# Performance work log

Measured on AMD Instinct MI355X. Metric: run time of the kernel, lower is better.

Reference implementation:

```python
import jax, jax.numpy as jnp
import numpy as np

B = 32
T, F1, F2 = 128, 8, 8          # input_shape
N_PATCHES = 1024               # (128/4)*(8/1)*(8/2)
INPUT_D = 8                    # 4*1*2
D = 64                         # hidden_d
H = 8                          # n_heads
DH = D // H                    # d_head = 8
S = N_PATCHES + 1              # sequence length with class token
OUT_D = 9
EPS = 1e-5


def _pos_emb(seq_len, d):
    # Faithful to the original (including the odd-index formula precedence):
    # even j: sin(i / 10000**(j/d));  odd j: cos(i / (10000**(j-1) / d))
    i = np.arange(seq_len, dtype=np.float64)[:, None]
    j = np.arange(d, dtype=np.float64)[None, :]
    even = np.sin(i / np.power(10000.0, j / d))
    odd = np.cos(i / (np.power(10000.0, j - 1.0) / d))
    return jnp.asarray(np.where(j.astype(np.int64) % 2 == 0, even, odd), dtype=jnp.float32)


def _layernorm2d(x, gamma, beta):
    # nn.LayerNorm((S, D)): normalize over the last TWO dims, affine [S, D]
    mu = jnp.mean(x, axis=(-2, -1), keepdims=True)
    var = jnp.mean((x - mu) ** 2, axis=(-2, -1), keepdims=True)
    return (x - mu) * jax.lax.rsqrt(var + EPS) * gamma + beta


def setup_inputs() -> dict:
    key = jax.random.key(0)
    ks = jax.random.split(key, 18)
    sc = 0.05
    return {
        "images": jax.random.normal(ks[0], (B, T, F1, F2), jnp.float32),
        "w_map": jax.random.normal(ks[1], (INPUT_D, D), jnp.float32) * sc,
        "b_map": jax.random.normal(ks[2], (D,), jnp.float32) * sc,
        "cls_tok": jax.random.uniform(ks[3], (1, D), jnp.float32),
        "g1": jnp.ones((S, D), jnp.float32),
        "be1": jnp.zeros((S, D), jnp.float32),
        "wq": jax.random.normal(ks[4], (H, DH, DH), jnp.float32) * sc,
        "bq": jax.random.normal(ks[5], (H, DH), jnp.float32) * sc,
        "wk": jax.random.normal(ks[6], (H, DH, DH), jnp.float32) * sc,
        "bk": jax.random.normal(ks[7], (H, DH), jnp.float32) * sc,
        "wv": jax.random.normal(ks[8], (H, DH, DH), jnp.float32) * sc,
        "bv": jax.random.normal(ks[9], (H, DH), jnp.float32) * sc,
        "g2": jnp.ones((S, D), jnp.float32),
        "be2": jnp.zeros((S, D), jnp.float32),
        "w_enc": jax.random.normal(ks[10], (D, D), jnp.float32) * sc,
        "b_enc": jax.random.normal(ks[11], (D,), jnp.float32) * sc,
        "w_out": jax.random.normal(ks[12], (D, OUT_D), jnp.float32) * sc,
        "b_out": jax.random.normal(ks[13], (OUT_D,), jnp.float32) * sc,
    }


def _msa(x, wq, bq, wk, bk, wv, bv):
    # x: [B, S, D] -> per-head linear QKV, softmax attention, concat heads
    b, s, _ = x.shape
    xh = x.reshape(b, s, H, DH)                                   # [B,S,H,dh]
    q = jnp.einsum("bshd,hde->bshe", xh, wq) + bq
    k = jnp.einsum("bshd,hde->bshe", xh, wk) + bk
    v = jnp.einsum("bshd,hde->bshe", xh, wv) + bv
    scores = jnp.einsum("bqhe,bkhe->bhqk", q, k) / (DH ** 0.5)    # [B,H,S,S]
    attn = jax.nn.softmax(scores, axis=-1)
    out = jnp.einsum("bhqk,bkhe->bqhe", attn, v)                  # [B,S,H,dh]
    return out.reshape(b, s, D)


def reference(images, w_map, b_map, cls_tok, g1, be1, wq, bq, wk, bk, wv, bv,
              g2, be2, w_enc, b_enc, w_out, b_out):
    n = images.shape[0]
    patches = images.reshape(n, N_PATCHES, INPUT_D)
    tokens = patches @ w_map + b_map                              # [B,P,D]
    cls = jnp.broadcast_to(cls_tok[None, :, :], (n, 1, D))
    tokens = jnp.concatenate([cls, tokens], axis=1)               # [B,S,D]
    tokens = tokens + _pos_emb(S, D)[None, :, :]
    out = tokens + _msa(_layernorm2d(tokens, g1, be1), wq, bq, wk, bk, wv, bv)
    out = out + jax.nn.relu(_layernorm2d(out, g2, be2) @ w_enc + b_enc)
    h = out[:, 0]                                                 # class token
    return jax.nn.softmax(h @ w_out + b_out, axis=-1)
```

## Files before the change

### kernel.cpp

```cpp
#include <hip/hip_runtime.h>
#include <math.h>

#define BB 32
#define SS 1025
#define DD 64
#define HH 8
#define IN_D 8
#define NPATCH 1024
#define OUTD 9
#define EPSF 1e-5f
#define SD (SS*DD)
#define SP 1056
#define NQT 65
#define NCH 33
#define VTROW 1064
#define PSTR 40
#define NTB 257
#define ZROW 1055

typedef __attribute__((ext_vector_type(8))) short bf16x8;
typedef __attribute__((ext_vector_type(4))) float f32x4;

#define SCALE_LOG2E (0.35355339059327378f * 1.4426950408889634f)

#if __has_builtin(__builtin_amdgcn_exp2f)
__device__ __forceinline__ float exp2_fast(float x) { return __builtin_amdgcn_exp2f(x); }
#else
__device__ __forceinline__ float exp2_fast(float x) {
    float r; asm("v_exp_f32 %0, %1" : "=v"(r) : "v"(x)); return r;
}
#endif

__device__ __forceinline__ short f2bf(float f) {
    union { float f; unsigned u; } a; a.f = f;
    unsigned r = a.u + 0x7FFFu + ((a.u >> 16) & 1u);
    return (short)(r >> 16);
}
__device__ __forceinline__ unsigned pack_bf16x2(float lo, float hi) {
    unsigned ul = __float_as_uint(lo) + 0x8000u;
    unsigned uh = __float_as_uint(hi) + 0x8000u;
    return __builtin_amdgcn_perm(uh, ul, 0x07060302u);
}

__device__ __forceinline__ int sigma32(int k) {
    return 16 * (k & 1) + 4 * (k >> 3) + ((k >> 1) & 3);
}

__global__ void k_tokens(const float* __restrict__ images, const float* __restrict__ w_map,
                         const float* __restrict__ b_map, const float* __restrict__ cls,
                         float* __restrict__ tokens, float* __restrict__ part1,
                         float* __restrict__ partq1, float* __restrict__ sum2,
                         float* __restrict__ sumsq2) {
    int b = blockIdx.y;
    int bx = blockIdx.x;
    int idx = bx * 256 + threadIdx.x;
    int tid = threadIdx.x;
    __shared__ float recip[64];
    __shared__ float sh[512];
    if (tid < 64) {
        int j = tid;
        float div;
        if ((j & 1) == 0)
            div = powf(10000.0f, (float)j * (1.0f / 64.0f));
        else
            div = powf(10000.0f, (float)(j - 1)) * (1.0f / 64.0f);
        recip[j] = 1.0f / div;
    }
    __syncthreads();
    float lv = 0.f, lvv = 0.f;
    if (idx < SD) {
        int s = idx >> 6, j = idx & 63;
        float arg = (float)s * recip[j];
        float pv = (j & 1) ? __cosf(arg) : __sinf(arg);
        float v;
        if (s == 0) {
            v = cls[j];
        } else {
            const float* p = images + (size_t)b * (NPATCH * IN_D) + (size_t)(s - 1) * IN_D;
            float acc = b_map[j];
#pragma unroll
            for (int i = 0; i < IN_D; ++i) acc += p[i] * w_map[i * DD + j];
            v = acc;
        }
        v += pv;
        tokens[(size_t)b * SD + idx] = v;
        lv = v; lvv = v * v;
    }
    sh[tid] = lv; sh[256 + tid] = lvv;
    __syncthreads();
    for (int off = 128; off > 0; off >>= 1) {
        if (tid < off) { sh[tid] += sh[tid + off]; sh[256 + tid] += sh[256 + tid + off]; }
        __syncthreads();
    }
    if (tid == 0) {
        part1[b * NTB + bx] = sh[0];
        partq1[b * NTB + bx] = sh[256];
    }
    if (bx == 0) {
        if (tid == 0) sum2[b] = 0.f;
        if (tid == 1) sumsq2[b] = 0.f;
    }
}

__global__ void k_qkv(const float* __restrict__ tokens, const float* __restrict__ part1,
                      const float* __restrict__ partq1, const float* __restrict__ g1,
                      const float* __restrict__ be1,
                      const float* __restrict__ wq, const float* __restrict__ bq,
                      const float* __restrict__ wk, const float* __restrict__ bk,
                      const float* __restrict__ wv, const float* __restrict__ bv,
                      short* __restrict__ qb, short* __restrict__ kb, short* __restrict__ vb) {
    int b = blockIdx.y, bx = blockIdx.x, tid = threadIdx.x;
    __shared__ float sh[512];
    __shared__ float xs[4][DD];
    __shared__ float stats[2];
    {
        float s = 0.f, ss = 0.f;
        for (int i = tid; i < NTB; i += 256) { s += part1[b * NTB + i]; ss += partq1[b * NTB + i]; }
        sh[tid] = s; sh[256 + tid] = ss;
        __syncthreads();
        for (int off = 128; off > 0; off >>= 1) {
            if (tid < off) { sh[tid] += sh[tid + off]; sh[256 + tid] += sh[256 + tid + off]; }
            __syncthreads();
        }
        if (tid == 0) {
            float mu = sh[0] / (float)SD;
            float var = sh[256] / (float)SD - mu * mu;
            stats[0] = mu;
            stats[1] = rsqrtf(var + EPSF);
        }
        __syncthreads();
    }
    int r = tid >> 6, d = tid & 63;
    int srow = bx * 4 + r;
    if (srow < SS) {
        float t = tokens[((size_t)b * SS + srow) * DD + d];
        xs[r][d] = (t - stats[0]) * stats[1] * g1[srow * DD + d] + be1[srow * DD + d];
    }
    __syncthreads();
    for (int o = tid; o < 768; o += 256) {
        int rr = o / 192;
        int rem = o % 192;
        int which = rem / 64;
        int he = rem % 64;
        int h = he >> 3, e = he & 7;
        int s2 = bx * 4 + rr;
        if (s2 >= SS) continue;
        const float* w = (which == 0) ? wq : (which == 1) ? wk : wv;
        const float* bias = (which == 0) ? bq : (which == 1) ? bk : bv;
        float acc = bias[he];
#pragma unroll
        for (int dd = 0; dd < 8; ++dd)
            acc += xs[rr][h * 8 + dd] * w[(h * 8 + dd) * 8 + e];
        if (which == 0) acc *= SCALE_LOG2E;
        short* dst = (which == 0) ? qb : (which == 1) ? kb : vb;
        dst[((size_t)(b * HH + h) * SP + s2) * 8 + e] = f2bf(acc);
    }
    if (bx == NTB - 1) {
        for (int i = tid; i < (SP - SS) * HH * 8; i += 256) {
            int rr = i / (HH * 8);
            int he = i % (HH * 8);
            int hh = he >> 3, e = he & 7;
            kb[((size_t)(b * HH + hh) * SP + SS + rr) * 8 + e] = 0;
        }
    }
}

__global__ __launch_bounds__(512, 6)
void k_attn(const short* __restrict__ qb, const short* __restrict__ kb, const short* __restrict__ vb,
            const float* __restrict__ tokens, float* __restrict__ out0,
            float* __restrict__ sum2, float* __restrict__ sumsq2) {
    __shared__ __align__(16) short VTs[9 * VTROW];
    __shared__ __align__(16) short Ps[8 * 2 * 16 * PSTR];
    int h = blockIdx.y, b = blockIdx.z;
    int bh = b * HH + h;
    int tid = threadIdx.x;
    int wave = tid >> 6, lane = tid & 63;
    int col = lane & 15, quad = lane >> 4;

    bf16x8 z8 = {0, 0, 0, 0, 0, 0, 0, 0};
    {
        const bf16x8* vg = (const bf16x8*)(vb + (size_t)bh * SP * 8);
        for (int i = tid; i < SP; i += 512) {
            int t = (i & ~31) | sigma32(i & 31);
            if (t < SS) {
                bf16x8 row = vg[t];
#pragma unroll
                for (int e = 0; e < 8; ++e) VTs[e * VTROW + i] = row[e];
                VTs[8 * VTROW + i] = (short)0x3F80;
            } else {
#pragma unroll
                for (int e = 0; e < 9; ++e) VTs[e * VTROW + i] = 0;
            }
        }
    }
    __syncthreads();

    const short* kg = kb + (size_t)bh * SP * 8;
    const short* kp0 = kg + ((quad == 0) ? col * 8 : ZROW * 8);
    const int kstep = (quad == 0) ? 256 : 0;
    const int koff16 = (quad == 0) ? 128 : 0;
    const short* vbase_l = VTs + (col < 9 ? col : 8) * VTROW + quad * 8;
    short* pbase = Ps + wave * (2 * 16 * PSTR);
    short* pwr = pbase + (quad * 4) * PSTR + 2 * col;
    const short* prd = pbase + col * PSTR + quad * 8;

    float lsum = 0.f, lssq = 0.f;
    int slot = blockIdx.x * 8 + wave;

    for (int qt = slot; qt < NQT; qt += 24) {
        bf16x8 qfrag = z8;
        if (quad == 0) qfrag = *(const bf16x8*)(qb + ((size_t)bh * SP + qt * 16 + col) * 8);
        f32x4 o = {0.f, 0.f, 0.f, 0.f};
        const f32x4 zz = {0.f, 0.f, 0.f, 0.f};
        const short* kptr = kp0;
        bf16x8 ka = *(const bf16x8*)kptr;
        bf16x8 kb_ = *(const bf16x8*)(kptr + koff16);
        {
            f32x4 s0 = __builtin_amdgcn_mfma_f32_16x16x32_bf16(qfrag, ka, zz, 0, 0, 0);
            f32x4 s1 = __builtin_amdgcn_mfma_f32_16x16x32_bf16(qfrag, kb_, zz, 0, 0, 0);
#pragma unroll
            for (int r = 0; r < 4; ++r)
                *(unsigned*)(pwr + r * PSTR) = pack_bf16x2(exp2_fast(s0[r]), exp2_fast(s1[r]));
        }
        for (int ch = 0; ch < NCH; ++ch) {
            bf16x8 pf = *(const bf16x8*)(prd + (ch & 1) * (16 * PSTR));
            bf16x8 vf = *(const bf16x8*)(vbase_l + ch * 32);
            if (ch + 1 < NCH) {
                kptr += kstep;
                ka = *(const bf16x8*)kptr;
                kb_ = *(const bf16x8*)(kptr + koff16);
                f32x4 s0 = __builtin_amdgcn_mfma_f32_16x16x32_bf16(qfrag, ka, zz, 0, 0, 0);
                f32x4 s1 = __builtin_amdgcn_mfma_f32_16x16x32_bf16(qfrag, kb_, zz, 0, 0, 0);
                short* pw = pwr + ((ch + 1) & 1) * (16 * PSTR);
#pragma unroll
                for (int r = 0; r < 4; ++r)
                    *(unsigned*)(pw + r * PSTR) = pack_bf16x2(exp2_fast(s0[r]), exp2_fast(s1[r]));
            }
            o = __builtin_amdgcn_mfma_f32_16x16x32_bf16(pf, vf, o, 0, 0, 0);
        }
        float* Pf = (float*)pbase;
#pragma unroll
        for (int r = 0; r < 4; ++r) Pf[(quad * 4 + r) * 16 + col] = o[r];
#pragma unroll
        for (int pass = 0; pass < 2; ++pass) {
            int idx = lane + pass * 64;
            int qq = idx >> 3, e = idx & 7;
            int qg = qt * 16 + qq;
            if (qg < SS) {
                float num = Pf[qq * 16 + e];
                float l = Pf[qq * 16 + 8];
                float ov = tokens[((size_t)b * SS + qg) * DD + h * 8 + e] + num / l;
                lsum += ov; lssq += ov * ov;
                if (qg == 0) out0[b * DD + h * 8 + e] = ov;
            }
        }
    }

    __syncthreads();
    float* red = (float*)Ps;
    red[tid] = lsum; red[512 + tid] = lssq;
    __syncthreads();
    for (int off = 256; off > 0; off >>= 1) {
        if (tid < off) { red[tid] += red[tid + off]; red[512 + tid] += red[512 + tid + off]; }
        __syncthreads();
    }
    if (tid == 0) {
        atomicAdd(&sum2[b], red[0]);
        atomicAdd(&sumsq2[b], red[512]);
    }
}

__global__ void k_final(const float* __restrict__ out0, const float* __restrict__ sum2,
                        const float* __restrict__ sumsq2, const float* __restrict__ g2,
                        const float* __restrict__ be2, const float* __restrict__ w_enc,
                        const float* __restrict__ b_enc, const float* __restrict__ w_out,
                        const float* __restrict__ b_out, float* __restrict__ out) {
    int b = blockIdx.x;
    int tid = threadIdx.x;
    __shared__ float xn[DD], hsh[DD], logit[OUTD];
    float n = (float)SD;
    float mu = sum2[b] / n;
    float var = sumsq2[b] / n - mu * mu;
    float rs = rsqrtf(var + EPSF);
    float o = out0[b * DD + tid];
    xn[tid] = (o - mu) * rs * g2[tid] + be2[tid];
    __syncthreads();
    float acc = b_enc[tid];
#pragma unroll
    for (int d = 0; d < DD; ++d) acc += xn[d] * w_enc[d * DD + tid];
    hsh[tid] = o + fmaxf(acc, 0.f);
    __syncthreads();
    if (tid < OUTD) {
        float a = b_out[tid];
#pragma unroll
        for (int d = 0; d < DD; ++d) a += hsh[d] * w_out[d * OUTD + tid];
        logit[tid] = a;
    }
    __syncthreads();
    if (tid == 0) {
        float m = logit[0];
        for (int i = 1; i < OUTD; ++i) m = fmaxf(m, logit[i]);
        float p[OUTD]; float ssum = 0.f;
        for (int i = 0; i < OUTD; ++i) { p[i] = expf(logit[i] - m); ssum += p[i]; }
        for (int i = 0; i < OUTD; ++i) out[b * OUTD + i] = p[i] / ssum;
    }
}

extern "C" void kernel_launch(void* const* d_in, const int* in_sizes, int n_in,
                              void* d_out, int out_size, void* d_ws, size_t ws_size,
                              hipStream_t stream) {
    const float* images = (const float*)d_in[0];
    const float* w_map  = (const float*)d_in[1];
    const float* b_map  = (const float*)d_in[2];
    const float* cls    = (const float*)d_in[3];
    const float* g1     = (const float*)d_in[4];
    const float* be1    = (const float*)d_in[5];
    const float* wq     = (const float*)d_in[6];
    const float* bq     = (const float*)d_in[7];
    const float* wk     = (const float*)d_in[8];
    const float* bk     = (const float*)d_in[9];
    const float* wv     = (const float*)d_in[10];
    const float* bv     = (const float*)d_in[11];
    const float* g2     = (const float*)d_in[12];
    const float* be2    = (const float*)d_in[13];
    const float* w_enc  = (const float*)d_in[14];
    const float* b_enc  = (const float*)d_in[15];
    const float* w_out  = (const float*)d_in[16];
    const float* b_out  = (const float*)d_in[17];
    float* out = (float*)d_out;

    float* ws = (float*)d_ws;
    size_t off = 0;
    float* tokens = ws + off; off += (size_t)BB * SD;
    float* out0   = ws + off; off += BB * DD;
    float* part1  = ws + off; off += BB * NTB;
    float* partq1 = ws + off; off += BB * NTB;
    float* sum2   = ws + off; off += BB;
    float* sumsq2 = ws + off; off += BB;
    short* qb = (short*)(ws + off); off += (size_t)BB * HH * SP * 8 / 2;
    short* kb = (short*)(ws + off); off += (size_t)BB * HH * SP * 8 / 2;
    short* vb = (short*)(ws + off); off += (size_t)BB * HH * SP * 8 / 2;

    k_tokens<<<dim3(NTB, BB), 256, 0, stream>>>(images, w_map, b_map, cls, tokens,
                                                part1, partq1, sum2, sumsq2);
    k_qkv<<<dim3(NTB, BB), 256, 0, stream>>>(tokens, part1, partq1, g1, be1,
                                             wq, bq, wk, bk, wv, bv, qb, kb, vb);
    k_attn<<<dim3(3, HH, BB), 512, 0, stream>>>(qb, kb, vb, tokens, out0, sum2, sumsq2);
    k_final<<<BB, DD, 0, stream>>>(out0, sum2, sumsq2, g2, be2, w_enc, b_enc, w_out, b_out, out);
}
```

Baseline: 181.9 us.

## Keep attention probabilities in registers by transposing the QK MFMA

Swaps the operand order of the score MFMA so each lane's S^T output already matches the A-operand layout needed for the P·V MFMA. The exponentiated probabilities are packed with v_cvt_pk_bf16_f32 and fed straight into the PV MFMA, which removes the per-chunk LDS write/read round trip and its double buffering. The V permutation in shared memory is changed to match the new key ordering. In exchange, the one-chunk software pipelining of exp against the PV MFMA is dropped, and bf16 rounding switches to the hardware convert.

```diff
diff --git a/kernel.cpp b/kernel.cpp
--- a/kernel.cpp
+++ b/kernel.cpp
@@ -14,7 +14,6 @@
 #define NQT 65
 #define NCH 33
 #define VTROW 1064
-#define PSTR 40
 #define NTB 257
 #define ZROW 1055
 
@@ -36,14 +35,15 @@
     unsigned r = a.u + 0x7FFFu + ((a.u >> 16) & 1u);
     return (short)(r >> 16);
 }
-__device__ __forceinline__ unsigned pack_bf16x2(float lo, float hi) {
-    unsigned ul = __float_as_uint(lo) + 0x8000u;
-    unsigned uh = __float_as_uint(hi) + 0x8000u;
-    return __builtin_amdgcn_perm(uh, ul, 0x07060302u);
-}
-
-__device__ __forceinline__ int sigma32(int k) {
-    return 16 * (k & 1) + 4 * (k >> 3) + ((k >> 1) & 3);
+
+__device__ __forceinline__ unsigned cvt_pk_bf16(float lo, float hi) {
+    unsigned r;
+    asm("v_cvt_pk_bf16_f32 %0, %1, %2" : "=v"(r) : "v"(lo), "v"(hi));
+    return r;
+}
+
+__device__ __forceinline__ int sigmaPV(int v) {
+    return ((v & 24) >> 1) | (v & 3) | ((v & 4) << 2);
 }
 
 __global__ void k_tokens(const float* __restrict__ images, const float* __restrict__ w_map,
@@ -170,7 +170,7 @@
             const float* __restrict__ tokens, float* __restrict__ out0,
             float* __restrict__ sum2, float* __restrict__ sumsq2) {
     __shared__ __align__(16) short VTs[9 * VTROW];
-    __shared__ __align__(16) short Ps[8 * 2 * 16 * PSTR];
+    __shared__ __align__(16) float Es[8 * 256];
     int h = blockIdx.y, b = blockIdx.z;
     int bh = b * HH + h;
     int tid = threadIdx.x;
@@ -181,7 +181,7 @@
     {
         const bf16x8* vg = (const bf16x8*)(vb + (size_t)bh * SP * 8);
         for (int i = tid; i < SP; i += 512) {
-            int t = (i & ~31) | sigma32(i & 31);
+            int t = (i & ~31) | sigmaPV(i & 31);
             if (t < SS) {
                 bf16x8 row = vg[t];
 #pragma unroll
@@ -200,9 +200,7 @@
     const int kstep = (quad == 0) ? 256 : 0;
     const int koff16 = (quad == 0) ? 128 : 0;
     const short* vbase_l = VTs + (col < 9 ? col : 8) * VTROW + quad * 8;
-    short* pbase = Ps + wave * (2 * 16 * PSTR);
-    short* pwr = pbase + (quad * 4) * PSTR + 2 * col;
-    const short* prd = pbase + col * PSTR + quad * 8;
+    float* Ef = Es + wave * 256;
 
     float lsum = 0.f, lssq = 0.f;
     int slot = blockIdx.x * 8 + wave;
@@ -215,40 +213,32 @@
         const short* kptr = kp0;
         bf16x8 ka = *(const bf16x8*)kptr;
         bf16x8 kb_ = *(const bf16x8*)(kptr + koff16);
-        {
-            f32x4 s0 = __builtin_amdgcn_mfma_f32_16x16x32_bf16(qfrag, ka, zz, 0, 0, 0);
-            f32x4 s1 = __builtin_amdgcn_mfma_f32_16x16x32_bf16(qfrag, kb_, zz, 0, 0, 0);
-#pragma unroll
-            for (int r = 0; r < 4; ++r)
-                *(unsigned*)(pwr + r * PSTR) = pack_bf16x2(exp2_fast(s0[r]), exp2_fast(s1[r]));
-        }
         for (int ch = 0; ch < NCH; ++ch) {
-            bf16x8 pf = *(const bf16x8*)(prd + (ch & 1) * (16 * PSTR));
             bf16x8 vf = *(const bf16x8*)(vbase_l + ch * 32);
+            f32x4 s0 = __builtin_amdgcn_mfma_f32_16x16x32_bf16(ka, qfrag, zz, 0, 0, 0);
+            f32x4 s1 = __builtin_amdgcn_mfma_f32_16x16x32_bf16(kb_, qfrag, zz, 0, 0, 0);
             if (ch + 1 < NCH) {
                 kptr += kstep;
                 ka = *(const bf16x8*)kptr;
                 kb_ = *(const bf16x8*)(kptr + koff16);
-                f32x4 s0 = __builtin_amdgcn_mfma_f32_16x16x32_bf16(qfrag, ka, zz, 0, 0, 0);
-                f32x4 s1 = __builtin_amdgcn_mfma_f32_16x16x32_bf16(qfrag, kb_, zz, 0, 0, 0);
-                short* pw = pwr + ((ch + 1) & 1) * (16 * PSTR);
-#pragma unroll
-                for (int r = 0; r < 4; ++r)
-                    *(unsigned*)(pw + r * PSTR) = pack_bf16x2(exp2_fast(s0[r]), exp2_fast(s1[r]));
             }
-            o = __builtin_amdgcn_mfma_f32_16x16x32_bf16(pf, vf, o, 0, 0, 0);
-        }
-        float* Pf = (float*)pbase;
-#pragma unroll
-        for (int r = 0; r < 4; ++r) Pf[(quad * 4 + r) * 16 + col] = o[r];
+            union { unsigned u[4]; bf16x8 v; } pa;
+            pa.u[0] = cvt_pk_bf16(exp2_fast(s0[0]), exp2_fast(s0[1]));
+            pa.u[1] = cvt_pk_bf16(exp2_fast(s0[2]), exp2_fast(s0[3]));
+            pa.u[2] = cvt_pk_bf16(exp2_fast(s1[0]), exp2_fast(s1[1]));
+            pa.u[3] = cvt_pk_bf16(exp2_fast(s1[2]), exp2_fast(s1[3]));
+            o = __builtin_amdgcn_mfma_f32_16x16x32_bf16(pa.v, vf, o, 0, 0, 0);
+        }
+#pragma unroll
+        for (int r = 0; r < 4; ++r) Ef[(quad * 4 + r) * 16 + col] = o[r];
 #pragma unroll
         for (int pass = 0; pass < 2; ++pass) {
             int idx = lane + pass * 64;
             int qq = idx >> 3, e = idx & 7;
             int qg = qt * 16 + qq;
             if (qg < SS) {
-                float num = Pf[qq * 16 + e];
-                float l = Pf[qq * 16 + 8];
+                float num = Ef[qq * 16 + e];
+                float l = Ef[qq * 16 + 8];
                 float ov = tokens[((size_t)b * SS + qg) * DD + h * 8 + e] + num / l;
                 lsum += ov; lssq += ov * ov;
                 if (qg == 0) out0[b * DD + h * 8 + e] = ov;
@@ -257,16 +247,15 @@
     }
 
     __syncthreads();
-    float* red = (float*)Ps;
-    red[tid] = lsum; red[512 + tid] = lssq;
+    Es[tid] = lsum; Es[512 + tid] = lssq;
     __syncthreads();
     for (int off = 256; off > 0; off >>= 1) {
-        if (tid < off) { red[tid] += red[tid + off]; red[512 + tid] += red[512 + tid + off]; }
+        if (tid < off) { Es[tid] += Es[tid + off]; Es[512 + tid] += Es[512 + tid + off]; }
         __syncthreads();
     }
     if (tid == 0) {
-        atomicAdd(&sum2[b], red[0]);
-        atomicAdd(&sumsq2[b], red[512]);
+        atomicAdd(&sum2[b], Es[0]);
+        atomicAdd(&sumsq2[b], Es[512]);
     }
 }
 
```

New measurement: 262.6 us. +44.4%, slower.
